# Kernel optimization log

Hardware: AMD Instinct MI355X
Metric: run time of the kernel (lower is better)

## Reference

```python
import jax, jax.numpy as jnp
import numpy as np

N_HEAD = 16
D_HEAD = 64
D_MODEL = 1024
N_ROLL = 3
SCALE = 1.0 / (D_HEAD ** 0.5)
EPS = 1e-5


def mul_roll_repeat(x, n_roll):
    # concat of x * roll(x, i) over i=1..n_roll along last dim
    return jnp.concatenate([x * jnp.roll(x, i, axis=-1) for i in range(1, n_roll + 1)], axis=-1)


def dpfp(x):
    # DPFP feature map: [relu(x), relu(-x)] then roll-multiply-repeat
    x2 = jnp.concatenate([jax.nn.relu(x), jax.nn.relu(-x)], axis=-1)
    return mul_roll_repeat(x2, N_ROLL)


def layer_norm(x, gamma, beta):
    mu = jnp.mean(x, axis=-1, keepdims=True)
    var = jnp.var(x, axis=-1, keepdims=True)
    return (x - mu) * jax.lax.rsqrt(var + 1e-5) * gamma + beta


def setup_inputs() -> dict:
    key = jax.random.key(0)
    ks = jax.random.split(key, 4)
    S, B = 2048, 2
    h = jax.random.normal(ks[0], (S, B, D_MODEL), dtype=jnp.float32)
    Wq = jax.random.normal(ks[1], (D_MODEL, N_HEAD * D_HEAD), dtype=jnp.float32) * 0.02
    Wkv = jax.random.normal(ks[2], (D_MODEL, 2 * N_HEAD * D_HEAD), dtype=jnp.float32) * 0.02
    Wo = jax.random.normal(ks[3], (N_HEAD * D_HEAD, D_MODEL), dtype=jnp.float32) * 0.02
    ln_gamma = jnp.ones((D_MODEL,), dtype=jnp.float32)
    ln_beta = jnp.zeros((D_MODEL,), dtype=jnp.float32)
    return {"h": h, "Wq": Wq, "Wkv": Wkv, "Wo": Wo, "ln_gamma": ln_gamma, "ln_beta": ln_beta}


def reference(h, Wq, Wkv, Wo, ln_gamma, ln_beta):
    # h: [S, B, D_MODEL]; mems=None, attn_mask=None, post-LN, eval (no dropout)
    S, B, _ = h.shape
    q = (h @ Wq).reshape(S, B, N_HEAD, D_HEAD)
    kv = h @ Wkv
    k, v = jnp.split(kv, 2, axis=-1)
    k = k.reshape(S, B, N_HEAD, D_HEAD)
    v = v.reshape(S, B, N_HEAD, D_HEAD)

    pq = dpfp(q)  # [S, B, N, F], F = 2*D_HEAD*N_ROLL = 384
    pk = dpfp(k)

    # Linear-attention form: identical math to the original quadratic
    # einsum('ibnd,jbnd->ijbn') * scale, summed over j for the denominator,
    # since there is no mask and dropatt=0. Avoids the O(S^2) score tensor.
    kv_agg = jnp.einsum('jbnf,jbnd->bnfd', pk, v)          # [B, N, F, D]
    z = pk.sum(axis=0)                                      # [B, N, F]
    num = jnp.einsum('ibnf,bnfd->ibnd', pq, kv_agg) * SCALE  # [S, B, N, D]
    den = jnp.einsum('ibnf,bnf->ibn', pq, z) * SCALE + EPS   # [S, B, N]
    attn_vec = (num / den[..., None]).reshape(S, B, N_HEAD * D_HEAD)

    attn_out = attn_vec @ Wo
    return layer_norm(h + attn_out, ln_gamma, ln_beta)
```

## Files before the change

kernel.cpp:

```cpp
#include <hip/hip_runtime.h>
#include <math.h>

#define NH 16
#define DM 1024
#define FEAT 384
#define SB 4096
#define SEQ 2048

static constexpr float SCALE = 0.125f;
static constexpr float EPS = 1e-5f;

typedef __attribute__((ext_vector_type(8))) _Float16 half8;
typedef __attribute__((ext_vector_type(4))) _Float16 half4;
typedef __attribute__((ext_vector_type(4))) float f32x4;

#define AS1 __attribute__((address_space(1)))
#define AS3 __attribute__((address_space(3)))

#define IDX(r, o) ((((r) << 6)) + ((((o) ^ ((r) & 7))) << 3))

__global__ __launch_bounds__(256) void prep_kernel(const float* __restrict__ h,
                                                   const float* __restrict__ Wq,
                                                   const float* __restrict__ Wkv,
                                                   const float* __restrict__ Wo,
                                                   _Float16* __restrict__ h_h,
                                                   _Float16* __restrict__ WqkvT,
                                                   _Float16* __restrict__ WoT) {
    __shared__ _Float16 tile[32][33];
    int bid = blockIdx.x, t = threadIdx.x;
    if (bid < 4096) {
        int i = bid * 256 + t;
        const float4 v = ((const float4*)h)[i];
        half4 o = {(_Float16)v.x, (_Float16)v.y, (_Float16)v.z, (_Float16)v.w};
        ((half4*)h_h)[i] = o;
        return;
    }
    const float* src;
    _Float16* dst;
    int N, col0, n0, k0;
    if (bid < 7168) {
        int b2 = bid - 4096;
        n0 = (b2 % 96) * 32; k0 = (b2 / 96) * 32;
        if (n0 < 1024) { src = Wq; N = 1024; col0 = n0; }
        else           { src = Wkv; N = 2048; col0 = n0 - 1024; }
        dst = WqkvT;
    } else {
        int b3 = bid - 7168;
        n0 = (b3 & 31) * 32; k0 = (b3 >> 5) * 32;
        src = Wo; N = 1024; col0 = n0; dst = WoT;
    }
    int tx = t & 31, ty = t >> 5;
    #pragma unroll
    for (int i = 0; i < 4; ++i)
        tile[ty + i * 8][tx] = (_Float16)src[(size_t)(k0 + ty + i * 8) * N + col0 + tx];
    __syncthreads();
    #pragma unroll
    for (int i = 0; i < 4; ++i)
        dst[(size_t)(n0 + ty + i * 8) * 1024 + k0 + tx] = tile[tx][ty + i * 8];
}

template <int MH>
__device__ __forceinline__ void mfma_all(f32x4 (&acc)[8][3], half8 (&a)[4][2],
                                         half8 (&bv)[3][2]) {
    #pragma unroll
    for (int mf = 0; mf < 4; ++mf)
        #pragma unroll
        for (int nf = 0; nf < 3; ++nf)
            #pragma unroll
            for (int ks = 0; ks < 2; ++ks)
                acc[MH * 4 + mf][nf] = __builtin_amdgcn_mfma_f32_16x16x32_f16(
                    a[mf][ks], bv[nf][ks], acc[MH * 4 + mf][nf], 0, 0, 0);
}

__global__ __launch_bounds__(512) void gemm_f16_8ph(const _Float16* __restrict__ A,
                                                    const _Float16* __restrict__ BT,
                                                    _Float16* __restrict__ C,
                                                    int M, int N, int K) {
    __shared__ _Float16 smem[57344];
    const int t = threadIdx.x;
    const int w = t >> 6, l = t & 63;
    const int wr = w >> 2, wc = w & 3;
    const int NT = K >> 6;
    const int NU = K >> 4;

    int nwg = gridDim.x;
    int cpx = nwg >> 3;
    int bid = blockIdx.x;
    int swz = (bid & 7) * cpx + (bid >> 3);
    int ntile = N / 192;
    int row0 = (swz / ntile) << 8;
    int col0 = (swz % ntile) * 192;

    f32x4 acc[8][3];
    #pragma unroll
    for (int m = 0; m < 8; ++m)
        #pragma unroll
        for (int n = 0; n < 3; ++n)
            acc[m][n] = (f32x4){0.f, 0.f, 0.f, 0.f};

    const int lr = l >> 3;
    const int lc8 = ((l & 7) ^ lr) * 8;

    auto STAGE = [&](int s) {
        if (s >= NU) return;
        int tau = s >> 2, u = s & 3;
        int kk = tau << 6;
        int bufo = (tau & 1) * 28672;
        if (u == 0) {
            #pragma unroll
            for (int i = 0; i < 2; ++i) {
                int chunk = w * 2 + i;
                const _Float16* src = BT + (size_t)(col0 + chunk * 8 + lr) * K + kk + lc8;
                __builtin_amdgcn_global_load_lds((const AS1 void*)src,
                    (AS3 void*)(smem + bufo + 16384 + chunk * 512), 16, 0, 0);
            }
        } else if (u == 1) {
            const _Float16* src = BT + (size_t)(col0 + 128 + w * 8 + lr) * K + kk + lc8;
            __builtin_amdgcn_global_load_lds((const AS1 void*)src,
                (AS3 void*)(smem + bufo + 24576 + w * 512), 16, 0, 0);
        } else {
            int rbase = (u == 3) ? 128 : 0;
            int lbase = (u == 3) ? 8192 : 0;
            #pragma unroll
            for (int i = 0; i < 2; ++i) {
                int chunk = w * 2 + i;
                const _Float16* src = A + (size_t)(row0 + rbase + chunk * 8 + lr) * K + kk + lc8;
                __builtin_amdgcn_global_load_lds((const AS1 void*)src,
                    (AS3 void*)(smem + bufo + lbase + chunk * 512), 16, 0, 0);
            }
        }
    };

    half8 a[4][2], bv[3][2];
    auto LDA = [&](int mh, int bufo) {
        #pragma unroll
        for (int mf = 0; mf < 4; ++mf) {
            int r = wr * 128 + (mh * 4 + mf) * 16 + (l & 15);
            #pragma unroll
            for (int ks = 0; ks < 2; ++ks) {
                int c16 = (ks * 4 + (l >> 4)) ^ (r & 7);
                a[mf][ks] = *(const half8*)&smem[bufo + r * 64 + c16 * 8];
            }
        }
    };
    auto LDB = [&](int bufo) {
        #pragma unroll
        for (int nf = 0; nf < 3; ++nf) {
            int r = wc * 48 + nf * 16 + (l & 15);
            #pragma unroll
            for (int ks = 0; ks < 2; ++ks) {
                int c16 = (ks * 4 + (l >> 4)) ^ (r & 7);
                bv[nf][ks] = *(const half8*)&smem[bufo + 16384 + r * 64 + c16 * 8];
            }
        }
    };

    STAGE(0); STAGE(1);
    STAGE(2); STAGE(3);
    STAGE(4); STAGE(5);
    asm volatile("s_waitcnt vmcnt(3)" ::: "memory");
    __builtin_amdgcn_s_barrier();

    #pragma unroll 1
    for (int ti = 0; ti < NT; ++ti) {
        const int bufo = (ti & 1) * 28672;
        const int sb = (ti + 1) << 2;
        LDA(0, bufo); LDB(bufo);
        STAGE(sb + 2); STAGE(sb + 3);
        __builtin_amdgcn_sched_barrier(0);
        __builtin_amdgcn_s_barrier();
        asm volatile("s_waitcnt lgkmcnt(0)" ::: "memory");
        __builtin_amdgcn_sched_barrier(0);
        __builtin_amdgcn_s_setprio(1);
        mfma_all<0>(acc, a, bv);
        __builtin_amdgcn_s_setprio(0);
        __builtin_amdgcn_sched_barrier(0);
        __builtin_amdgcn_s_barrier();
        LDA(1, bufo);
        STAGE(sb + 4); STAGE(sb + 5);
        __builtin_amdgcn_sched_barrier(0);
        __builtin_amdgcn_s_barrier();
        asm volatile("s_waitcnt lgkmcnt(0)" ::: "memory");
        __builtin_amdgcn_sched_barrier(0);
        __builtin_amdgcn_s_setprio(1);
        mfma_all<1>(acc, a, bv);
        __builtin_amdgcn_s_setprio(0);
        __builtin_amdgcn_sched_barrier(0);
        if (ti < NT - 2) asm volatile("s_waitcnt vmcnt(3)" ::: "memory");
        else             asm volatile("s_waitcnt vmcnt(0)" ::: "memory");
        __builtin_amdgcn_s_barrier();
    }

    int ocol = l & 15, orow4 = (l >> 4) * 4;
    #pragma unroll
    for (int mf = 0; mf < 8; ++mf)
        #pragma unroll
        for (int nf = 0; nf < 3; ++nf) {
            size_t base = (size_t)(row0 + wr * 128 + mf * 16 + orow4) * N
                        + col0 + wc * 48 + nf * 16 + ocol;
            #pragma unroll
            for (int j = 0; j < 4; ++j)
                C[base + (size_t)j * N] = (_Float16)acc[mf][nf][j];
        }
}

__global__ __launch_bounds__(256) void gemm_wo(const _Float16* __restrict__ A,
                                               const _Float16* __restrict__ BT,
                                               _Float16* __restrict__ C,
                                               int M, int N, int K) {
    __shared__ _Float16 smem[3 * 16384];
    const int t = threadIdx.x;
    const int w = t >> 6, l = t & 63;
    const int wr = w >> 1, wc = w & 1;
    const int NT = K >> 6;
    int row0 = blockIdx.y * 128, col0 = blockIdx.x * 128;

    f32x4 acc[4][4];
    #pragma unroll
    for (int m = 0; m < 4; ++m)
        #pragma unroll
        for (int n = 0; n < 4; ++n)
            acc[m][n] = (f32x4){0.f, 0.f, 0.f, 0.f};

    const int lr = l >> 3;
    const int lc8 = ((l & 7) ^ lr) * 8;

    auto STAGE = [&](int ti) {
        if (ti >= NT) return;
        int kk = ti << 6;
        int bufo = (ti % 3) * 16384;
        #pragma unroll
        for (int i = 0; i < 4; ++i) {
            int chunk = w * 4 + i;
            const _Float16* asrc = A + (size_t)(row0 + chunk * 8 + lr) * K + kk + lc8;
            __builtin_amdgcn_global_load_lds((const AS1 void*)asrc,
                (AS3 void*)(smem + bufo + chunk * 512), 16, 0, 0);
            const _Float16* bsrc = BT + (size_t)(col0 + chunk * 8 + lr) * K + kk + lc8;
            __builtin_amdgcn_global_load_lds((const AS1 void*)bsrc,
                (AS3 void*)(smem + bufo + 8192 + chunk * 512), 16, 0, 0);
        }
    };

    STAGE(0); STAGE(1);
    asm volatile("s_waitcnt vmcnt(8)" ::: "memory");
    __builtin_amdgcn_s_barrier();

    #pragma unroll 1
    for (int ti = 0; ti < NT; ++ti) {
        const int bufo = (ti % 3) * 16384;
        half8 a[4][2], bv[4][2];
        #pragma unroll
        for (int mf = 0; mf < 4; ++mf) {
            int r = wr * 64 + mf * 16 + (l & 15);
            #pragma unroll
            for (int ks = 0; ks < 2; ++ks) {
                int c16 = (ks * 4 + (l >> 4)) ^ (r & 7);
                a[mf][ks] = *(const half8*)&smem[bufo + r * 64 + c16 * 8];
            }
        }
        #pragma unroll
        for (int nf = 0; nf < 4; ++nf) {
            int r = wc * 64 + nf * 16 + (l & 15);
            #pragma unroll
            for (int ks = 0; ks < 2; ++ks) {
                int c16 = (ks * 4 + (l >> 4)) ^ (r & 7);
                bv[nf][ks] = *(const half8*)&smem[bufo + 8192 + r * 64 + c16 * 8];
            }
        }
        STAGE(ti + 2);
        __builtin_amdgcn_sched_barrier(0);
        asm volatile("s_waitcnt lgkmcnt(0)" ::: "memory");
        __builtin_amdgcn_sched_barrier(0);
        __builtin_amdgcn_s_setprio(1);
        #pragma unroll
        for (int mf = 0; mf < 4; ++mf)
            #pragma unroll
            for (int nf = 0; nf < 4; ++nf)
                #pragma unroll
                for (int ks = 0; ks < 2; ++ks)
                    acc[mf][nf] = __builtin_amdgcn_mfma_f32_16x16x32_f16(
                        a[mf][ks], bv[nf][ks], acc[mf][nf], 0, 0, 0);
        __builtin_amdgcn_s_setprio(0);
        __builtin_amdgcn_sched_barrier(0);
        if (ti < NT - 2) asm volatile("s_waitcnt vmcnt(8)" ::: "memory");
        else             asm volatile("s_waitcnt vmcnt(0)" ::: "memory");
        __builtin_amdgcn_s_barrier();
    }

    int ocol = l & 15, orow = (l >> 4) * 4;
    #pragma unroll
    for (int mf = 0; mf < 4; ++mf)
        #pragma unroll
        for (int nf = 0; nf < 4; ++nf) {
            size_t base = (size_t)(row0 + wr * 64 + mf * 16 + orow) * N
                        + col0 + wc * 64 + nf * 16 + ocol;
            #pragma unroll
            for (int j = 0; j < 4; ++j)
                C[base + (size_t)j * N] = (_Float16)acc[mf][nf][j];
        }
}

__global__ __launch_bounds__(512) void kvagg_fused(const _Float16* __restrict__ qkv,
                                                   _Float16* __restrict__ kvp,
                                                   float* __restrict__ zp) {
    __shared__ _Float16 x2s[128 * 64];
    __shared__ _Float16 vTs[64 * 64];
    __shared__ _Float16 pkTs[384 * 64];
    const int t = threadIdx.x;
    const int w = t >> 6, l = t & 63;
    const int bn = blockIdx.x;
    const int jseg = blockIdx.y;
    const int b = bn >> 4, nh = bn & 15;

    f32x4 acc[4][3];
    #pragma unroll
    for (int mf = 0; mf < 4; ++mf)
        #pragma unroll
        for (int nf = 0; nf < 3; ++nf)
            acc[mf][nf] = (f32x4){0.f, 0.f, 0.f, 0.f};
    float zacc[3] = {0.f, 0.f, 0.f};

    const int sc = t & 63;
    const int so = t >> 6;

    #pragma unroll 1
    for (int ch = 0; ch < 4; ++ch) {
        int j0 = jseg * 256 + ch * 64;
        _Float16 kx[8], vx[8];
        #pragma unroll
        for (int e = 0; e < 8; ++e) {
            size_t rb = (size_t)((j0 + so * 8 + e) * 2 + b) * 3072 + nh * 64 + sc;
            kx[e] = qkv[rb + 1024];
            vx[e] = qkv[rb + 2048];
        }
        half8 xlo, xhi, vv;
        #pragma unroll
        for (int e = 0; e < 8; ++e) {
            float kf = (float)kx[e];
            xlo[e] = (_Float16)fmaxf(kf, 0.f);
            xhi[e] = (_Float16)fmaxf(-kf, 0.f);
            vv[e] = vx[e];
        }
        if (ch) __syncthreads();
        *(half8*)&x2s[IDX(sc, so)] = xlo;
        *(half8*)&x2s[IDX(sc + 64, so)] = xhi;
        *(half8*)&vTs[IDX(sc, so)] = vv;
        __syncthreads();
        {
            const int o = t & 7;
            const int fb = t >> 3;
            #pragma unroll
            for (int it = 0; it < 6; ++it) {
                int f = it * 64 + fb;
                int fm = f & 127;
                int r = (f >> 7) + 1;
                int fm2 = (fm - r) & 127;
                half8 pa = *(const half8*)&x2s[IDX(fm, o)];
                half8 pb = *(const half8*)&x2s[IDX(fm2, o)];
                *(half8*)&pkTs[IDX(f, o)] = pa * pb;
            }
        }
        __syncthreads();
        #pragma unroll
        for (int ks = 0; ks < 2; ++ks) {
            half8 a[4], bq[3];
            int oo = ks * 4 + (l >> 4);
            #pragma unroll
            for (int mf = 0; mf < 4; ++mf) {
                int dr = mf * 16 + (l & 15);
                a[mf] = *(const half8*)&vTs[IDX(dr, oo)];
            }
            #pragma unroll
            for (int nf = 0; nf < 3; ++nf) {
                int fr = w * 48 + nf * 16 + (l & 15);
                bq[nf] = *(const half8*)&pkTs[IDX(fr, oo)];
                #pragma unroll
                for (int e = 0; e < 8; ++e) zacc[nf] += (float)bq[nf][e];
            }
            #pragma unroll
            for (int mf = 0; mf < 4; ++mf)
                #pragma unroll
                for (int nf = 0; nf < 3; ++nf)
                    acc[mf][nf] = __builtin_amdgcn_mfma_f32_16x16x32_f16(
                        a[mf], bq[nf], acc[mf][nf], 0, 0, 0);
        }
    }

    #pragma unroll
    for (int nf = 0; nf < 3; ++nf) {
        float v = zacc[nf];
        v += __shfl_xor(v, 16, 64);
        v += __shfl_xor(v, 32, 64);
        if (l < 16)
            zp[(size_t)(jseg * 32 + bn) * FEAT + w * 48 + nf * 16 + l] = v;
    }
    _Float16* outp = kvp + (size_t)(jseg * 32 + bn) * 64 * FEAT;
    int orow = (l >> 4) * 4, ocol = l & 15;
    #pragma unroll
    for (int mf = 0; mf < 4; ++mf)
        #pragma unroll
        for (int nf = 0; nf < 3; ++nf) {
            int fcol = w * 48 + nf * 16 + ocol;
            #pragma unroll
            for (int j = 0; j < 4; ++j)
                outp[(size_t)(mf * 16 + orow + j) * FEAT + fcol] = (_Float16)acc[mf][nf][j];
        }
}

__global__ __launch_bounds__(256) void reduceA(const _Float16* __restrict__ kvp,
                                               const float* __restrict__ zp,
                                               _Float16* __restrict__ kvaggT,
                                               float* __restrict__ z) {
    const int NKV = 32 * 64 * FEAT;
    int idx = blockIdx.x * 256 + threadIdx.x;
    if (idx < NKV) {
        float s = 0.f;
        #pragma unroll
        for (int c = 0; c < 8; ++c) s += (float)kvp[(size_t)c * NKV + idx];
        kvaggT[idx] = (_Float16)s;
    } else if (idx < NKV + 32 * FEAT) {
        int e = idx - NKV;
        float s = 0.f;
        #pragma unroll
        for (int c = 0; c < 8; ++c) s += zp[c * 32 * FEAT + e];
        z[e] = s;
    }
}

#define X2STR 152
__global__ __launch_bounds__(256) void attn_fused(const _Float16* __restrict__ qkv,
                                                  const _Float16* __restrict__ kvaggT,
                                                  const float* __restrict__ z,
                                                  _Float16* __restrict__ av) {
    __shared__ _Float16 x2e[64 * X2STR];
    __shared__ _Float16 B_lds[64 * FEAT];
    __shared__ float z_lds[FEAT];
    __shared__ float den_lds[64];
    const int t = threadIdx.x;
    const int w = t >> 6, l = t & 63;
    const int iblk = blockIdx.x;
    const int bn = blockIdx.y;
    const int b = bn >> 4, nh = bn & 15;

    {
        const _Float16* Bg = kvaggT + (size_t)bn * 64 * FEAT;
        #pragma unroll
        for (int s = 0; s < 12; ++s) {
            int idx8 = t + 256 * s;
            int row = idx8 / 48, c16 = idx8 - row * 48;
            half8 vv = *(const half8*)&Bg[row * FEAT + c16 * 8];
            *(half8*)&B_lds[row * FEAT + ((c16 ^ (row & 7)) << 3)] = vv;
        }
    }
    for (int e = t; e < FEAT; e += 256) z_lds[e] = z[(size_t)bn * FEAT + e];

    {
        int row = t >> 2, c0 = (t & 3) * 16;
        const _Float16* qrow = qkv + (size_t)((iblk * 64 + row) * 2 + b) * 3072 + nh * 64;
        half8 q0 = *(const half8*)&qrow[c0];
        half8 q1 = *(const half8*)&qrow[c0 + 8];
        half8 lo0, lo1, hi0, hi1;
        #pragma unroll
        for (int e = 0; e < 8; ++e) {
            float f0 = (float)q0[e], f1 = (float)q1[e];
            lo0[e] = (_Float16)fmaxf(f0, 0.f);
            lo1[e] = (_Float16)fmaxf(f1, 0.f);
            hi0[e] = (_Float16)fmaxf(-f0, 0.f);
            hi1[e] = (_Float16)fmaxf(-f1, 0.f);
        }
        _Float16* xr = &x2e[row * X2STR];
        *(half8*)&xr[c0] = lo0;
        *(half8*)&xr[c0 + 8] = lo1;
        *(half8*)&xr[64 + c0] = hi0;
        *(half8*)&xr[64 + c0 + 8] = hi1;
        if (c0 == 0) { *(half8*)&xr[128] = lo0; *(half8*)&xr[136] = lo1; }
        if (c0 == 16) { *(half8*)&xr[144] = lo0; }
    }
    __syncthreads();

    const int rloc16 = l & 15;
    const int csel = (l >> 4) * 8;
    const int lrow = w * 16 + rloc16;
    half8 y8[16];
    {
        const _Float16* xr = &x2e[lrow * X2STR + csel];
        #pragma unroll
        for (int j = 0; j < 16; ++j)
            y8[j] = *(const half8*)&xr[j * 8];
    }
    half8 afr[12];
    #pragma unroll
    for (int ks = 0; ks < 12; ++ks) {
        const int r = (ks >> 2) + 1;
        #pragma unroll
        for (int e = 0; e < 8; ++e) {
            const int j1 = ((ks & 3) * 32 + e) & 127;
            const int j2 = ((ks & 3) * 32 + e - r) & 127;
            afr[ks][e] = y8[j1 >> 3][j1 & 7] * y8[j2 >> 3][j2 & 7];
        }
    }

    f32x4 acc[4];
    #pragma unroll
    for (int n = 0; n < 4; ++n) acc[n] = (f32x4){0.f, 0.f, 0.f, 0.f};
    float den = 0.f;
    #pragma unroll
    for (int ks = 0; ks < 12; ++ks) {
        #pragma unroll
        for (int e = 0; e < 8; ++e)
            den += (float)afr[ks][e] * z_lds[ks * 32 + csel + e];
        #pragma unroll
        for (int nf = 0; nf < 4; ++nf) {
            int row = nf * 16 + rloc16;
            int c16 = (ks * 4 + (l >> 4)) ^ (row & 7);
            half8 bfr = *(const half8*)&B_lds[row * FEAT + (c16 << 3)];
            acc[nf] = __builtin_amdgcn_mfma_f32_16x16x32_f16(afr[ks], bfr, acc[nf], 0, 0, 0);
        }
    }

    den += __shfl_xor(den, 16, 64);
    den += __shfl_xor(den, 32, 64);
    if (l < 16) den_lds[w * 16 + l] = den;
    __syncthreads();

    #pragma unroll
    for (int nf = 0; nf < 4; ++nf)
        #pragma unroll
        for (int j = 0; j < 4; ++j) {
            int rl = w * 16 + (l >> 4) * 4 + j;
            float dv = den_lds[rl] * SCALE + EPS;
            float val = acc[nf][j] * SCALE / dv;
            int i = iblk * 64 + rl;
            av[((size_t)i * 2 + b) * 1024 + nh * 64 + nf * 16 + (l & 15)] = (_Float16)val;
        }
}

__global__ __launch_bounds__(256) void ln_kernel(const float* __restrict__ h,
                                                 const _Float16* __restrict__ attn_out,
                                                 const float* __restrict__ gamma,
                                                 const float* __restrict__ beta,
                                                 float* __restrict__ out) {
    int r = blockIdx.x;
    int t = threadIdx.x;
    const float4 hv = ((const float4*)(h + (size_t)r * 1024))[t];
    const half4 a4 = ((const half4*)(attn_out + (size_t)r * 1024))[t];
    float x[4] = {hv.x + (float)a4[0], hv.y + (float)a4[1],
                  hv.z + (float)a4[2], hv.w + (float)a4[3]};
    float sum = x[0] + x[1] + x[2] + x[3];
    float sq = x[0]*x[0] + x[1]*x[1] + x[2]*x[2] + x[3]*x[3];
    #pragma unroll
    for (int off = 32; off >= 1; off >>= 1) {
        sum += __shfl_xor(sum, off, 64);
        sq += __shfl_xor(sq, off, 64);
    }
    __shared__ float ssum[4], ssq[4];
    int wl = t >> 6, lane = t & 63;
    if (lane == 0) { ssum[wl] = sum; ssq[wl] = sq; }
    __syncthreads();
    sum = ssum[0] + ssum[1] + ssum[2] + ssum[3];
    sq = ssq[0] + ssq[1] + ssq[2] + ssq[3];
    float mu = sum * (1.f / 1024.f);
    float var = sq * (1.f / 1024.f) - mu * mu;
    float rs = rsqrtf(var + 1e-5f);
    const float4 g4 = ((const float4*)gamma)[t];
    const float4 b4 = ((const float4*)beta)[t];
    float4 o;
    o.x = (x[0] - mu) * rs * g4.x + b4.x;
    o.y = (x[1] - mu) * rs * g4.y + b4.y;
    o.z = (x[2] - mu) * rs * g4.z + b4.z;
    o.w = (x[3] - mu) * rs * g4.w + b4.w;
    ((float4*)(out + (size_t)r * 1024))[t] = o;
}

extern "C" void kernel_launch(void* const* d_in, const int* in_sizes, int n_in,
                              void* d_out, int out_size, void* d_ws, size_t ws_size,
                              hipStream_t stream) {
    const float* h     = (const float*)d_in[0];
    const float* Wq    = (const float*)d_in[1];
    const float* Wkv   = (const float*)d_in[2];
    const float* Wo    = (const float*)d_in[3];
    const float* gamma = (const float*)d_in[4];
    const float* beta  = (const float*)d_in[5];
    float* out = (float*)d_out;
    _Float16* u = (_Float16*)d_ws;

    _Float16* h_h    = u;
    _Float16* WqkvT  = u + 4194304;
    _Float16* WoT    = u + 7340032;
    _Float16* qkv    = u + 8388608;
    _Float16* kvp    = u + 20971520;
    float*    zp     = (float*)(u + 33554432);
    _Float16* kvaggT = u + 33751040;
    float*    z      = (float*)(u + 34537472);
    _Float16* av         = h_h;
    _Float16* attn_out_h = qkv;

    dim3 blk(256);
    prep_kernel<<<dim3(8192), blk, 0, stream>>>(h, Wq, Wkv, Wo, h_h, WqkvT, WoT);
    gemm_f16_8ph<<<dim3(256), dim3(512), 0, stream>>>(h_h, WqkvT, qkv, SB, 3072, DM);
    kvagg_fused<<<dim3(32, 8), dim3(512), 0, stream>>>(qkv, kvp, zp);
    reduceA<<<dim3(3120), blk, 0, stream>>>(kvp, zp, kvaggT, z);
    attn_fused<<<dim3(32, 32), blk, 0, stream>>>(qkv, kvaggT, z, av);
    gemm_wo<<<dim3(8, 32), blk, 0, stream>>>(av, WoT, attn_out_h, SB, 1024, DM);
    ln_kernel<<<dim3(SB), blk, 0, stream>>>(h, attn_out_h, gamma, beta, out);
}
```

Before: 99.33 us.

## Simplify QKV GEMM to single-stage double buffering with 4x2 wave layout

Replaces the 8-phase staggered QKV GEMM pipeline, which split each K-tile load into four sub-stages interleaved across two MFMA halves, with a simpler scheme. Each iteration now prefetches the whole next K-tile, computes the current one, then waits on vmcnt(0) and barriers. Waves now form a 4x2 grid, each owning 64x96 outputs instead of 128x48, so A fragments are reused across six B fragments. Separately, the denominator dot product in the attention kernel reads z from LDS as float4 vectors. The simpler pipeline cuts barriers and code complexity but may expose more global-load latency, since loads can no longer overlap with finer-grained compute phases.

```diff
diff --git a/kernel.cpp b/kernel.cpp
--- a/kernel.cpp
+++ b/kernel.cpp
@@ -59,29 +59,15 @@
         dst[(size_t)(n0 + ty + i * 8) * 1024 + k0 + tx] = tile[tx][ty + i * 8];
 }
 
-template <int MH>
-__device__ __forceinline__ void mfma_all(f32x4 (&acc)[8][3], half8 (&a)[4][2],
-                                         half8 (&bv)[3][2]) {
-    #pragma unroll
-    for (int mf = 0; mf < 4; ++mf)
-        #pragma unroll
-        for (int nf = 0; nf < 3; ++nf)
-            #pragma unroll
-            for (int ks = 0; ks < 2; ++ks)
-                acc[MH * 4 + mf][nf] = __builtin_amdgcn_mfma_f32_16x16x32_f16(
-                    a[mf][ks], bv[nf][ks], acc[MH * 4 + mf][nf], 0, 0, 0);
-}
-
-__global__ __launch_bounds__(512) void gemm_f16_8ph(const _Float16* __restrict__ A,
-                                                    const _Float16* __restrict__ BT,
-                                                    _Float16* __restrict__ C,
-                                                    int M, int N, int K) {
+__global__ __launch_bounds__(512) void gemm_qkv(const _Float16* __restrict__ A,
+                                                const _Float16* __restrict__ BT,
+                                                _Float16* __restrict__ C,
+                                                int M, int N, int K) {
     __shared__ _Float16 smem[57344];
     const int t = threadIdx.x;
     const int w = t >> 6, l = t & 63;
-    const int wr = w >> 2, wc = w & 3;
+    const int wr = w >> 1, wc = w & 1;
     const int NT = K >> 6;
-    const int NU = K >> 4;
 
     int nwg = gridDim.x;
     int cpx = nwg >> 3;
@@ -91,113 +77,93 @@
     int row0 = (swz / ntile) << 8;
     int col0 = (swz % ntile) * 192;
 
-    f32x4 acc[8][3];
-    #pragma unroll
-    for (int m = 0; m < 8; ++m)
-        #pragma unroll
-        for (int n = 0; n < 3; ++n)
+    f32x4 acc[4][6];
+    #pragma unroll
+    for (int m = 0; m < 4; ++m)
+        #pragma unroll
+        for (int n = 0; n < 6; ++n)
             acc[m][n] = (f32x4){0.f, 0.f, 0.f, 0.f};
 
     const int lr = l >> 3;
     const int lc8 = ((l & 7) ^ lr) * 8;
 
-    auto STAGE = [&](int s) {
-        if (s >= NU) return;
-        int tau = s >> 2, u = s & 3;
+    auto STAGE_TILE = [&](int tau) {
+        if (tau >= NT) return;
         int kk = tau << 6;
         int bufo = (tau & 1) * 28672;
-        if (u == 0) {
-            #pragma unroll
-            for (int i = 0; i < 2; ++i) {
-                int chunk = w * 2 + i;
-                const _Float16* src = BT + (size_t)(col0 + chunk * 8 + lr) * K + kk + lc8;
-                __builtin_amdgcn_global_load_lds((const AS1 void*)src,
-                    (AS3 void*)(smem + bufo + 16384 + chunk * 512), 16, 0, 0);
-            }
-        } else if (u == 1) {
+        #pragma unroll
+        for (int i = 0; i < 2; ++i) {
+            int chunk = w * 2 + i;
+            const _Float16* src = BT + (size_t)(col0 + chunk * 8 + lr) * K + kk + lc8;
+            __builtin_amdgcn_global_load_lds((const AS1 void*)src,
+                (AS3 void*)(smem + bufo + 16384 + chunk * 512), 16, 0, 0);
+        }
+        {
             const _Float16* src = BT + (size_t)(col0 + 128 + w * 8 + lr) * K + kk + lc8;
             __builtin_amdgcn_global_load_lds((const AS1 void*)src,
                 (AS3 void*)(smem + bufo + 24576 + w * 512), 16, 0, 0);
-        } else {
-            int rbase = (u == 3) ? 128 : 0;
-            int lbase = (u == 3) ? 8192 : 0;
-            #pragma unroll
-            for (int i = 0; i < 2; ++i) {
-                int chunk = w * 2 + i;
-                const _Float16* src = A + (size_t)(row0 + rbase + chunk * 8 + lr) * K + kk + lc8;
-                __builtin_amdgcn_global_load_lds((const AS1 void*)src,
-                    (AS3 void*)(smem + bufo + lbase + chunk * 512), 16, 0, 0);
-            }
+        }
+        #pragma unroll
+        for (int i = 0; i < 4; ++i) {
+            int chunk = w * 4 + i;
+            const _Float16* src = A + (size_t)(row0 + chunk * 8 + lr) * K + kk + lc8;
+            __builtin_amdgcn_global_load_lds((const AS1 void*)src,
+                (AS3 void*)(smem + bufo + chunk * 512), 16, 0, 0);
         }
     };
 
-    half8 a[4][2], bv[3][2];
-    auto LDA = [&](int mh, int bufo) {
+    STAGE_TILE(0);
+    asm volatile("s_waitcnt vmcnt(0)" ::: "memory");
+    __builtin_amdgcn_s_barrier();
+
+    #pragma unroll 1
+    for (int ti = 0; ti < NT; ++ti) {
+        const int bufo = (ti & 1) * 28672;
+        STAGE_TILE(ti + 1);
+        half8 a[4][2], bv[6][2];
         #pragma unroll
         for (int mf = 0; mf < 4; ++mf) {
-            int r = wr * 128 + (mh * 4 + mf) * 16 + (l & 15);
+            int r = wr * 64 + mf * 16 + (l & 15);
             #pragma unroll
             for (int ks = 0; ks < 2; ++ks) {
                 int c16 = (ks * 4 + (l >> 4)) ^ (r & 7);
                 a[mf][ks] = *(const half8*)&smem[bufo + r * 64 + c16 * 8];
             }
         }
-    };
-    auto LDB = [&](int bufo) {
-        #pragma unroll
-        for (int nf = 0; nf < 3; ++nf) {
-            int r = wc * 48 + nf * 16 + (l & 15);
+        #pragma unroll
+        for (int nf = 0; nf < 6; ++nf) {
+            int r = wc * 96 + nf * 16 + (l & 15);
             #pragma unroll
             for (int ks = 0; ks < 2; ++ks) {
                 int c16 = (ks * 4 + (l >> 4)) ^ (r & 7);
                 bv[nf][ks] = *(const half8*)&smem[bufo + 16384 + r * 64 + c16 * 8];
             }
         }
-    };
-
-    STAGE(0); STAGE(1);
-    STAGE(2); STAGE(3);
-    STAGE(4); STAGE(5);
-    asm volatile("s_waitcnt vmcnt(3)" ::: "memory");
-    __builtin_amdgcn_s_barrier();
-
-    #pragma unroll 1
-    for (int ti = 0; ti < NT; ++ti) {
-        const int bufo = (ti & 1) * 28672;
-        const int sb = (ti + 1) << 2;
-        LDA(0, bufo); LDB(bufo);
-        STAGE(sb + 2); STAGE(sb + 3);
         __builtin_amdgcn_sched_barrier(0);
-        __builtin_amdgcn_s_barrier();
         asm volatile("s_waitcnt lgkmcnt(0)" ::: "memory");
         __builtin_amdgcn_sched_barrier(0);
         __builtin_amdgcn_s_setprio(1);
-        mfma_all<0>(acc, a, bv);
+        #pragma unroll
+        for (int mf = 0; mf < 4; ++mf)
+            #pragma unroll
+            for (int nf = 0; nf < 6; ++nf)
+                #pragma unroll
+                for (int ks = 0; ks < 2; ++ks)
+                    acc[mf][nf] = __builtin_amdgcn_mfma_f32_16x16x32_f16(
+                        a[mf][ks], bv[nf][ks], acc[mf][nf], 0, 0, 0);
         __builtin_amdgcn_s_setprio(0);
         __builtin_amdgcn_sched_barrier(0);
+        asm volatile("s_waitcnt vmcnt(0)" ::: "memory");
         __builtin_amdgcn_s_barrier();
-        LDA(1, bufo);
-        STAGE(sb + 4); STAGE(sb + 5);
-        __builtin_amdgcn_sched_barrier(0);
-        __builtin_amdgcn_s_barrier();
-        asm volatile("s_waitcnt lgkmcnt(0)" ::: "memory");
-        __builtin_amdgcn_sched_barrier(0);
-        __builtin_amdgcn_s_setprio(1);
-        mfma_all<1>(acc, a, bv);
-        __builtin_amdgcn_s_setprio(0);
-        __builtin_amdgcn_sched_barrier(0);
-        if (ti < NT - 2) asm volatile("s_waitcnt vmcnt(3)" ::: "memory");
-        else             asm volatile("s_waitcnt vmcnt(0)" ::: "memory");
-        __builtin_amdgcn_s_barrier();
     }
 
     int ocol = l & 15, orow4 = (l >> 4) * 4;
     #pragma unroll
-    for (int mf = 0; mf < 8; ++mf)
-        #pragma unroll
-        for (int nf = 0; nf < 3; ++nf) {
-            size_t base = (size_t)(row0 + wr * 128 + mf * 16 + orow4) * N
-                        + col0 + wc * 48 + nf * 16 + ocol;
+    for (int mf = 0; mf < 4; ++mf)
+        #pragma unroll
+        for (int nf = 0; nf < 6; ++nf) {
+            size_t base = (size_t)(row0 + wr * 64 + mf * 16 + orow4) * N
+                        + col0 + wc * 96 + nf * 16 + ocol;
             #pragma unroll
             for (int j = 0; j < 4; ++j)
                 C[base + (size_t)j * N] = (_Float16)acc[mf][nf][j];
@@ -506,9 +472,12 @@
     float den = 0.f;
     #pragma unroll
     for (int ks = 0; ks < 12; ++ks) {
-        #pragma unroll
-        for (int e = 0; e < 8; ++e)
-            den += (float)afr[ks][e] * z_lds[ks * 32 + csel + e];
+        const float4 z0 = *(const float4*)&z_lds[ks * 32 + csel];
+        const float4 z1 = *(const float4*)&z_lds[ks * 32 + csel + 4];
+        den += (float)afr[ks][0] * z0.x + (float)afr[ks][1] * z0.y
+             + (float)afr[ks][2] * z0.z + (float)afr[ks][3] * z0.w
+             + (float)afr[ks][4] * z1.x + (float)afr[ks][5] * z1.y
+             + (float)afr[ks][6] * z1.z + (float)afr[ks][7] * z1.w;
         #pragma unroll
         for (int nf = 0; nf < 4; ++nf) {
             int row = nf * 16 + rloc16;
@@ -597,7 +566,7 @@
 
     dim3 blk(256);
     prep_kernel<<<dim3(8192), blk, 0, stream>>>(h, Wq, Wkv, Wo, h_h, WqkvT, WoT);
-    gemm_f16_8ph<<<dim3(256), dim3(512), 0, stream>>>(h_h, WqkvT, qkv, SB, 3072, DM);
+    gemm_qkv<<<dim3(256), dim3(512), 0, stream>>>(h_h, WqkvT, qkv, SB, 3072, DM);
     kvagg_fused<<<dim3(32, 8), dim3(512), 0, stream>>>(qkv, kvp, zp);
     reduceA<<<dim3(3120), blk, 0, stream>>>(kvp, zp, kvaggT, z);
     attn_fused<<<dim3(32, 32), blk, 0, stream>>>(qkv, kvaggT, z, av);
```

Result: no change. 97.95 us, median of 3 (-1.4%).
